# Optimization experiments

Measured on AMD Instinct MI355X. Metric: run time of the kernel, lower is better.

The kernel has to match this reference:

```python
import jax, jax.numpy as jnp
import numpy as np

B, S, K = 4, 2048, 8
N_NEURONS, N_BASIS, RANK = 64, 32, 8
D_MODEL, D_HID = 256, 1024


def setup_inputs() -> dict:
    key = jax.random.key(0)
    ks = jax.random.split(key, 10)
    x = jax.random.normal(ks[0], (B, S, D_MODEL), dtype=jnp.float32)
    neuron_idx = jax.random.randint(ks[1], (B, S, K), 0, N_NEURONS)
    w = jax.random.uniform(ks[2], (B, S, K), dtype=jnp.float32)
    neuron_weights = w / jnp.sum(w, axis=-1, keepdims=True)  # softmax-like routing weights
    neuron_recipes = jax.random.normal(ks[3], (N_NEURONS, N_BASIS), dtype=jnp.float32) * 0.5
    sc = 0.1
    basis_A1 = jax.random.normal(ks[4], (N_BASIS, 16, RANK, 8), dtype=jnp.float32) * sc
    basis_A2 = jax.random.normal(ks[5], (N_BASIS, RANK, 16, 8), dtype=jnp.float32) * sc
    basis_B1 = jax.random.normal(ks[6], (N_BASIS, 8, RANK, 32), dtype=jnp.float32) * sc
    basis_B2 = jax.random.normal(ks[7], (N_BASIS, RANK, 8, 32), dtype=jnp.float32) * sc
    w_down_w = jax.random.normal(ks[8], (D_HID, D_MODEL), dtype=jnp.float32) * (1.0 / np.sqrt(D_HID))
    w_down_b = jnp.zeros((D_MODEL,), dtype=jnp.float32)
    return {
        "x": x, "neuron_idx": neuron_idx, "neuron_weights": neuron_weights,
        "neuron_recipes": neuron_recipes,
        "basis_A1": basis_A1, "basis_A2": basis_A2,
        "basis_B1": basis_B1, "basis_B2": basis_B2,
        "w_down_w": w_down_w, "w_down_b": w_down_b,
    }


def reference(x, neuron_idx, neuron_weights, neuron_recipes,
              basis_A1, basis_A2, basis_B1, basis_B2, w_down_w, w_down_b):
    Bt, St, D = x.shape
    # --- routing: gather recipes of selected neurons, softmax, weighted-combine ---
    sel = neuron_recipes[neuron_idx]                       # [B,S,k,n_basis]
    sel = jax.nn.softmax(sel, axis=-1)
    wr = jnp.einsum('bskn,bsk->bsn', sel, neuron_weights)  # [B,S,n_basis]
    # --- build per-token TT cores from basis banks (get_neuron_tt_cores) ---
    cA1 = jnp.einsum('bsn,nirk->bsirk', wr, basis_A1)      # [B,S,16,r,8]
    cA2 = jnp.einsum('bsn,nrjl->bsrjl', wr, basis_A2)      # [B,S,r,16,8]
    cB1 = jnp.einsum('bsn,nirk->bsirk', wr, basis_B1)      # [B,S,8,r,32]
    cB2 = jnp.einsum('bsn,nrjl->bsrjl', wr, basis_B2)      # [B,S,r,8,32]
    # --- TT FFN: 256 -> 64 ---
    x_fold = x.reshape(Bt, St, 16, 16)
    temp = jnp.einsum('bsij,bsirk->bsjrk', x_fold, cA1)
    h = jnp.einsum('bsjrk,bsrjl->bskl', temp, cA2).reshape(Bt, St, 64)
    # --- TT FFN: 64 -> 1024 ---
    h_fold = h.reshape(Bt, St, 8, 8)
    temp = jnp.einsum('bsij,bsirk->bsjrk', h_fold, cB1)
    out = jnp.einsum('bsjrk,bsrjl->bskl', temp, cB2).reshape(Bt, St, D_HID)
    out = jax.nn.gelu(out, approximate=False)              # torch F.gelu default = exact erf
    return out @ w_down_w + w_down_b                       # [B,S,256]
```

## Files before the change

### kernel.cpp

```cpp
#include <hip/hip_runtime.h>
#include <math.h>


typedef unsigned short u16;
typedef __attribute__((ext_vector_type(8))) __bf16 bf16x8;
typedef __attribute__((ext_vector_type(4))) float f32x4;
union ABCast { float4 f; bf16x8 v; };
union BFBits { __bf16 b; u16 u; };
union Pack8 { u16 u[8]; float4 f; };

__device__ __forceinline__ float gelu_exact(float v) {
    return 0.5f * v * (1.0f + erff(v * 0.70710678118654752440f));
}
__device__ __forceinline__ u16 f2bf_bits(float f) { BFBits c; c.b = (__bf16)f; return c.u; }
__device__ __forceinline__ float bfbits2f(u16 u) { BFBits c; c.u = u; return (float)c.b; }

__global__ __launch_bounds__(64) void k_route(
    const int* __restrict__ nidx, const float* __restrict__ nw,
    const float* __restrict__ recipes, float* __restrict__ wr_out,
    u16* __restrict__ wrAh, u16* __restrict__ wrAl)
{
    const int t = blockIdx.x * 64 + threadIdx.x;
    float acc[32];
#pragma unroll
    for (int n = 0; n < 32; n++) acc[n] = 0.f;
#pragma unroll
    for (int k = 0; k < 8; k++) {
        const int   id = nidx[t * 8 + k];
        const float wk = nw[t * 8 + k];
        const float4* row = (const float4*)(recipes + id * 32);
        float v[32];
#pragma unroll
        for (int q = 0; q < 8; q++) {
            float4 f = row[q];
            v[q*4+0] = f.x; v[q*4+1] = f.y; v[q*4+2] = f.z; v[q*4+3] = f.w;
        }
        float m = v[0];
#pragma unroll
        for (int n = 1; n < 32; n++) m = fmaxf(m, v[n]);
        float s = 0.f;
#pragma unroll
        for (int n = 0; n < 32; n++) { float e = expf(v[n] - m); v[n] = e; s += e; }
        const float iv = wk / s;
#pragma unroll
        for (int n = 0; n < 32; n++) acc[n] += v[n] * iv;
    }
    float4* o = (float4*)(wr_out + t * 32);
#pragma unroll
    for (int q = 0; q < 8; q++)
        o[q] = make_float4(acc[q*4+0], acc[q*4+1], acc[q*4+2], acc[q*4+3]);

    const int tg16 = t >> 4, tl = t & 15;
#pragma unroll
    for (int c = 0; c < 4; c++) {
        Pack8 ph, pl;
#pragma unroll
        for (int e = 0; e < 8; e++) {
            const float v = acc[c*8 + e];
            const u16 hb = f2bf_bits(v);
            ph.u[e] = hb;
            pl.u[e] = f2bf_bits(v - bfbits2f(hb));
        }
        const int lane = c * 16 + tl;
        *(float4*)(wrAh + (tg16*64 + lane)*8) = ph.f;
        *(float4*)(wrAl + (tg16*64 + lane)*8) = pl.f;
    }
}

__global__ __launch_bounds__(512) void k_stageA(
    const float* __restrict__ x, const float* __restrict__ wr,
    const float* __restrict__ A1, const float* __restrict__ A2,
    float* __restrict__ h_out)
{
    __shared__ float ca[8 * 1024];
    __shared__ float tl[8 * 1088];
    const int tid = threadIdx.x;
    const int t0  = blockIdx.x * 8;
    {
        const int e2 = tid * 2;
        float2 c[8];
#pragma unroll
        for (int tt = 0; tt < 8; tt++) c[tt] = make_float2(0.f, 0.f);
#pragma unroll 4
        for (int n = 0; n < 32; n++) {
            const float2 a = *(const float2*)(A1 + n * 1024 + e2);
#pragma unroll
            for (int tt = 0; tt < 8; tt++) {
                const float s = wr[(t0 + tt) * 32 + n];
                c[tt].x += s * a.x; c[tt].y += s * a.y;
            }
        }
#pragma unroll
        for (int tt = 0; tt < 8; tt++) *(float2*)(ca + tt * 1024 + e2) = c[tt];
    }
    __syncthreads();
    {
        const int t = tid >> 6, g = tid & 63, j = g >> 2, eh = g & 3;
        float xr[16];
#pragma unroll
        for (int i = 0; i < 16; i++) xr[i] = x[(t0 + t) * 256 + i * 16 + j];
        float tr[16];
#pragma unroll
        for (int q = 0; q < 16; q++) tr[q] = 0.f;
#pragma unroll
        for (int i = 0; i < 16; i++) {
            const float xv = xr[i];
#pragma unroll
            for (int q = 0; q < 4; q++) {
                const float4 cv = *(const float4*)(ca + t * 1024 + i * 64 + eh * 16 + q * 4);
                tr[q*4+0] += xv * cv.x; tr[q*4+1] += xv * cv.y;
                tr[q*4+2] += xv * cv.z; tr[q*4+3] += xv * cv.w;
            }
        }
#pragma unroll
        for (int q = 0; q < 4; q++)
            *(float4*)(tl + t * 1088 + j * 68 + eh * 16 + q * 4) =
                make_float4(tr[q*4+0], tr[q*4+1], tr[q*4+2], tr[q*4+3]);
    }
    __syncthreads();
    {
        const int e2 = tid * 2;
        float2 c[8];
#pragma unroll
        for (int tt = 0; tt < 8; tt++) c[tt] = make_float2(0.f, 0.f);
#pragma unroll 4
        for (int n = 0; n < 32; n++) {
            const float2 a = *(const float2*)(A2 + n * 1024 + e2);
#pragma unroll
            for (int tt = 0; tt < 8; tt++) {
                const float s = wr[(t0 + tt) * 32 + n];
                c[tt].x += s * a.x; c[tt].y += s * a.y;
            }
        }
#pragma unroll
        for (int tt = 0; tt < 8; tt++) *(float2*)(ca + tt * 1024 + e2) = c[tt];
    }
    __syncthreads();
    {
        const int t = tid >> 6, g = tid & 63, k = g >> 3, l = g & 7;
        float acc = 0.f;
#pragma unroll
        for (int j = 0; j < 16; j++) {
#pragma unroll
            for (int r = 0; r < 8; r++) {
                acc += tl[t * 1088 + j * 68 + r * 8 + k] *
                       ca[t * 1024 + r * 128 + j * 8 + l];
            }
        }
        h_out[(t0 + t) * 64 + g] = acc;
    }
}

__global__ __launch_bounds__(256) void k_bsplit(
    const float* __restrict__ B1, const float* __restrict__ B2,
    u16* __restrict__ o1h, u16* __restrict__ o1l,
    u16* __restrict__ o2h, u16* __restrict__ o2l)
{
    const int slot = blockIdx.x * 256 + threadIdx.x;
    const int bank = slot >> 13, r = (slot >> 10) & 7, g = (slot >> 6) & 15, l = slot & 63;
    const int c = l & 15, nb = 8 * (l >> 4);
    const int base = (bank == 0)
        ? ((g >> 1) * 256 + r * 32 + (g & 1) * 16 + c)
        : (r * 256 + (g >> 1) * 32 + (g & 1) * 16 + c);
    const float* S = (bank ? B2 : B1) + base + nb * 2048;
    Pack8 ph, pl;
#pragma unroll
    for (int e = 0; e < 8; e++) {
        const float v = S[e * 2048];
        const u16 hb = f2bf_bits(v);
        ph.u[e] = hb;
        pl.u[e] = f2bf_bits(v - bfbits2f(hb));
    }
    const int d = ((r * 16 + g) * 64 + l) * 8;
    *(float4*)((bank ? o2h : o1h) + d) = ph.f;
    *(float4*)((bank ? o2l : o1l) + d) = pl.f;
}

__global__ __launch_bounds__(256) void k_wsplit(
    const float* __restrict__ W, u16* __restrict__ wfh, u16* __restrict__ wfl)
{
    const int slot = blockIdx.x * 256 + threadIdx.x;
    const int ng = slot >> 11, kc = (slot >> 6) & 31, l = slot & 63;
    const float* S = W + (kc * 32 + 8 * (l >> 4)) * 256 + ng * 16 + (l & 15);
    Pack8 ph, pl;
#pragma unroll
    for (int e = 0; e < 8; e++) {
        const float v = S[e * 256];
        const u16 hb = f2bf_bits(v);
        ph.u[e] = hb;
        pl.u[e] = f2bf_bits(v - bfbits2f(hb));
    }
    const int d = ((ng * 32 + kc) * 64 + l) * 8;
    *(float4*)(wfh + d) = ph.f;
    *(float4*)(wfl + d) = pl.f;
}

__global__ __launch_bounds__(1024, 2) void k_fusedB(
    const float* __restrict__ hin,
    const u16* __restrict__ wrAh, const u16* __restrict__ wrAl,
    const u16* __restrict__ bf1h, const u16* __restrict__ bf1l,
    const u16* __restrict__ bf2h, const u16* __restrict__ bf2l,
    const u16* __restrict__ wfh, const u16* __restrict__ wfl,
    const float* __restrict__ bias, float* __restrict__ y)
{
    __shared__ __align__(16) unsigned char smem[65536];
    float* hs  = (float*)smem;
    float* cb1 = hs + 1024;
    float* cb2 = cb1 + 16 * 264;
    float* t2  = cb2 + 16 * 264;
    u16* gAh = (u16*)smem;
    u16* gAl = gAh + 16384;

    const int tid = threadIdx.x;
    const int l   = tid & 63;
    const int w   = tid >> 6;
    const int tg  = blockIdx.x;
    const int t0  = tg * 16;

    hs[tid] = hin[t0 * 64 + tid];

    ABCast cu;
    cu.f = *(const float4*)(wrAh + (tg * 64 + l) * 8); const bf16x8 wra_h = cu.v;
    cu.f = *(const float4*)(wrAl + (tg * 64 + l) * 8); const bf16x8 wra_l = cu.v;

    const bool isB2 = (w >= 8);
    const u16* bsrc_h = isB2 ? bf2h : bf1h;
    const u16* bsrc_l = isB2 ? bf2l : bf1l;
    float* cdst = isB2 ? cb2 : cb1;
    const int g0 = (w & 7) * 2;

    const int j2 = l >> 3, k42 = l & 7;
    const int k0 = (l & 7) * 4, l0 = (l >> 3) * 4;

    float hreg[8];
#pragma unroll
    for (int i = 0; i < 8; i++) hreg[i] = hs[w * 64 + i * 8 + j2];

    float o[4][4];
#pragma unroll
    for (int a = 0; a < 4; a++)
#pragma unroll
        for (int li = 0; li < 4; li++) o[a][li] = 0.f;

    float4 pbh0 = *(const float4*)(bsrc_h + ((g0 + 0)*64 + l)*8);
    float4 pbl0 = *(const float4*)(bsrc_l + ((g0 + 0)*64 + l)*8);
    float4 pbh1 = *(const float4*)(bsrc_h + ((g0 + 1)*64 + l)*8);
    float4 pbl1 = *(const float4*)(bsrc_l + ((g0 + 1)*64 + l)*8);

#pragma unroll 1
    for (int r = 0; r < 8; r++) {
        {
            ABCast ch, cl2;
            ch.f = pbh0; cl2.f = pbl0;
            f32x4 cc = {0.f, 0.f, 0.f, 0.f};
            cc = __builtin_amdgcn_mfma_f32_16x16x32_bf16(wra_h, ch.v,  cc, 0, 0, 0);
            cc = __builtin_amdgcn_mfma_f32_16x16x32_bf16(wra_h, cl2.v, cc, 0, 0, 0);
            cc = __builtin_amdgcn_mfma_f32_16x16x32_bf16(wra_l, ch.v,  cc, 0, 0, 0);
            {
                const int gg = g0;
                float* cd = cdst + (gg >> 1) * 32 + (gg & 1) * 16 + (l & 15);
#pragma unroll
                for (int reg = 0; reg < 4; reg++)
                    cd[(4 * (l >> 4) + reg) * 264] = cc[reg];
            }
            ch.f = pbh1; cl2.f = pbl1;
            f32x4 cc2 = {0.f, 0.f, 0.f, 0.f};
            cc2 = __builtin_amdgcn_mfma_f32_16x16x32_bf16(wra_h, ch.v,  cc2, 0, 0, 0);
            cc2 = __builtin_amdgcn_mfma_f32_16x16x32_bf16(wra_h, cl2.v, cc2, 0, 0, 0);
            cc2 = __builtin_amdgcn_mfma_f32_16x16x32_bf16(wra_l, ch.v,  cc2, 0, 0, 0);
            {
                const int gg = g0 + 1;
                float* cd = cdst + (gg >> 1) * 32 + (gg & 1) * 16 + (l & 15);
#pragma unroll
                for (int reg = 0; reg < 4; reg++)
                    cd[(4 * (l >> 4) + reg) * 264] = cc2[reg];
            }
        }
        if (r < 7) {
            const int rb = (r + 1) * 16;
            pbh0 = *(const float4*)(bsrc_h + ((rb + g0 + 0)*64 + l)*8);
            pbl0 = *(const float4*)(bsrc_l + ((rb + g0 + 0)*64 + l)*8);
            pbh1 = *(const float4*)(bsrc_h + ((rb + g0 + 1)*64 + l)*8);
            pbl1 = *(const float4*)(bsrc_l + ((rb + g0 + 1)*64 + l)*8);
        }
        __syncthreads();

        {
            float4 acc = make_float4(0.f, 0.f, 0.f, 0.f);
#pragma unroll
            for (int i = 0; i < 8; i++) {
                const float  hv = hreg[i];
                const float4 cv = *(const float4*)(cb1 + w * 264 + i * 32 + k42 * 4);
                acc.x += hv * cv.x; acc.y += hv * cv.y;
                acc.z += hv * cv.z; acc.w += hv * cv.w;
            }
            *(float4*)(t2 + w * 264 + j2 * 32 + k42 * 4) = acc;
        }

        {
#pragma unroll
            for (int j = 0; j < 8; j++) {
                const float4 tv4 = *(const float4*)(t2  + w * 264 + j * 32 + k0);
                const float4 cv4 = *(const float4*)(cb2 + w * 264 + j * 32 + l0);
                const float tv[4] = {tv4.x, tv4.y, tv4.z, tv4.w};
                const float cv[4] = {cv4.x, cv4.y, cv4.z, cv4.w};
#pragma unroll
                for (int a = 0; a < 4; a++)
#pragma unroll
                    for (int li = 0; li < 4; li++)
                        o[a][li] += tv[a] * cv[li];
            }
        }
        __syncthreads();
    }

    {
        const int lane2 = (l0 >> 3) * 16 + w;
        const int e0 = l0 & 7;
#pragma unroll
        for (int a = 0; a < 4; a++) {
            u16 hv[4], lv[4];
#pragma unroll
            for (int li = 0; li < 4; li++) {
                const float v = gelu_exact(o[a][li]);
                const u16 hb = f2bf_bits(v);
                hv[li] = hb;
                lv[li] = f2bf_bits(v - bfbits2f(hb));
            }
            const int step = k0 + a;
            *(ushort4*)(gAh + (step * 64 + lane2) * 8 + e0) = make_ushort4(hv[0], hv[1], hv[2], hv[3]);
            *(ushort4*)(gAl + (step * 64 + lane2) * 8 + e0) = make_ushort4(lv[0], lv[1], lv[2], lv[3]);
        }
    }
    __syncthreads();

    if (w < 8) {
        f32x4 dacc0 = {0.f, 0.f, 0.f, 0.f}, dacc1 = {0.f, 0.f, 0.f, 0.f};
        const int wb0 = w * 16384 + l * 8;
        const int wb1 = (w + 8) * 16384 + l * 8;
#pragma unroll 2
        for (int kc = 0; kc < 32; kc++) {
            cu.f = *(const float4*)(gAh + (kc * 64 + l) * 8); const bf16x8 ah = cu.v;
            cu.f = *(const float4*)(gAl + (kc * 64 + l) * 8); const bf16x8 al = cu.v;
            ABCast c0, c1, c2, c3;
            c0.f = *(const float4*)(wfh + wb0 + kc * 512); const bf16x8 bh0 = c0.v;
            c1.f = *(const float4*)(wfl + wb0 + kc * 512); const bf16x8 bl0 = c1.v;
            c2.f = *(const float4*)(wfh + wb1 + kc * 512); const bf16x8 bh1 = c2.v;
            c3.f = *(const float4*)(wfl + wb1 + kc * 512); const bf16x8 bl1 = c3.v;
            dacc0 = __builtin_amdgcn_mfma_f32_16x16x32_bf16(ah, bh0, dacc0, 0, 0, 0);
            dacc0 = __builtin_amdgcn_mfma_f32_16x16x32_bf16(ah, bl0, dacc0, 0, 0, 0);
            dacc0 = __builtin_amdgcn_mfma_f32_16x16x32_bf16(al, bh0, dacc0, 0, 0, 0);
            dacc1 = __builtin_amdgcn_mfma_f32_16x16x32_bf16(ah, bh1, dacc1, 0, 0, 0);
            dacc1 = __builtin_amdgcn_mfma_f32_16x16x32_bf16(ah, bl1, dacc1, 0, 0, 0);
            dacc1 = __builtin_amdgcn_mfma_f32_16x16x32_bf16(al, bh1, dacc1, 0, 0, 0);
        }
        const int n0 = w * 16 + (l & 15);
        const int n1 = (w + 8) * 16 + (l & 15);
        const float b0 = bias[n0], b1 = bias[n1];
        const int tb = t0 + 4 * (l >> 4);
#pragma unroll
        for (int reg = 0; reg < 4; reg++) {
            y[(tb + reg) * 256 + n0] = dacc0[reg] + b0;
            y[(tb + reg) * 256 + n1] = dacc1[reg] + b1;
        }
    }
}

extern "C" void kernel_launch(void* const* d_in, const int* in_sizes, int n_in,
                              void* d_out, int out_size, void* d_ws, size_t ws_size,
                              hipStream_t stream)
{
    const float* x    = (const float*)d_in[0];
    const int*   nidx = (const int*)  d_in[1];
    const float* nw   = (const float*)d_in[2];
    const float* rec  = (const float*)d_in[3];
    const float* A1   = (const float*)d_in[4];
    const float* A2   = (const float*)d_in[5];
    const float* B1   = (const float*)d_in[6];
    const float* B2   = (const float*)d_in[7];
    const float* Wd   = (const float*)d_in[8];
    const float* bd   = (const float*)d_in[9];
    float* y  = (float*)d_out;

    float* wr  = (float*)d_ws;
    float* h   = wr + 8192 * 32;
    u16* wrAh  = (u16*)(h + 8192 * 64);
    u16* wrAl  = wrAh + 262144;
    u16* b1h   = wrAl + 262144;
    u16* b1l   = b1h + 65536;
    u16* b2h   = b1l + 65536;
    u16* b2l   = b2h + 65536;
    u16* wfh   = b2l + 65536;
    u16* wfl   = wfh + 262144;

    k_route <<<128,  64,   0, stream>>>(nidx, nw, rec, wr, wrAh, wrAl);
    k_stageA<<<1024, 512,  0, stream>>>(x, wr, A1, A2, h);
    k_bsplit<<<64,   256,  0, stream>>>(B1, B2, b1h, b1l, b2h, b2l);
    k_wsplit<<<128,  256,  0, stream>>>(Wd, wfh, wfl);
    k_fusedB<<<512,  1024, 0, stream>>>(h, wrAh, wrAl, b1h, b1l, b2h, b2l, wfh, wfl, bd, y);
}
```

Measured before the change: 101.1 us.

## Double-buffer TT core build and compute t2 in registers to drop a barrier

Core tiles cb1/cb2 are now double-buffered in shared memory, so the MFMA build of the next rank slice overlaps with the contraction on the current one, leaving one barrier per iteration instead of two. The t2 intermediate is no longer staged through shared memory: each thread recomputes the full 8x4 slice it needs in registers from a per-wave copy of h held in 64 registers. This raises register pressure and redundant FMAs under launch_bounds(1024,2) and grows shared memory past 64KB, which may cost occupancy or cause spills.

```diff
diff --git a/kernel.cpp b/kernel.cpp
--- a/kernel.cpp
+++ b/kernel.cpp
@@ -203,11 +203,9 @@
     const u16* __restrict__ wfh, const u16* __restrict__ wfl,
     const float* __restrict__ bias, float* __restrict__ y)
 {
-    __shared__ __align__(16) unsigned char smem[65536];
-    float* hs  = (float*)smem;
-    float* cb1 = hs + 1024;
-    float* cb2 = cb1 + 16 * 264;
-    float* t2  = cb2 + 16 * 264;
+    __shared__ __align__(16) unsigned char smem[67584];
+    float* cb1 = (float*)smem;
+    float* cb2 = cb1 + 2 * 16 * 264;
     u16* gAh = (u16*)smem;
     u16* gAl = gAh + 16384;
 
@@ -217,7 +215,11 @@
     const int tg  = blockIdx.x;
     const int t0  = tg * 16;
 
-    hs[tid] = hin[t0 * 64 + tid];
+    const int wu = __builtin_amdgcn_readfirstlane(w);
+    const float* hp = hin + (t0 + wu) * 64;
+    float hsg[64];
+#pragma unroll
+    for (int q = 0; q < 64; q++) hsg[q] = hp[q];
 
     ABCast cu;
     cu.f = *(const float4*)(wrAh + (tg * 64 + l) * 8); const bf16x8 wra_h = cu.v;
@@ -226,93 +228,92 @@
     const bool isB2 = (w >= 8);
     const u16* bsrc_h = isB2 ? bf2h : bf1h;
     const u16* bsrc_l = isB2 ? bf2l : bf1l;
-    float* cdst = isB2 ? cb2 : cb1;
+    float* cdst0 = isB2 ? cb2 : cb1;
     const int g0 = (w & 7) * 2;
 
-    const int j2 = l >> 3, k42 = l & 7;
     const int k0 = (l & 7) * 4, l0 = (l >> 3) * 4;
 
-    float hreg[8];
-#pragma unroll
-    for (int i = 0; i < 8; i++) hreg[i] = hs[w * 64 + i * 8 + j2];
-
     float o[4][4];
 #pragma unroll
     for (int a = 0; a < 4; a++)
 #pragma unroll
         for (int li = 0; li < 4; li++) o[a][li] = 0.f;
 
-    float4 pbh0 = *(const float4*)(bsrc_h + ((g0 + 0)*64 + l)*8);
-    float4 pbl0 = *(const float4*)(bsrc_l + ((g0 + 0)*64 + l)*8);
-    float4 pbh1 = *(const float4*)(bsrc_h + ((g0 + 1)*64 + l)*8);
-    float4 pbl1 = *(const float4*)(bsrc_l + ((g0 + 1)*64 + l)*8);
+    float4 pbh0, pbl0, pbh1, pbl1;
+#define LOADB(R) {                                                              \
+    const int rb_ = (R) * 16;                                                   \
+    pbh0 = *(const float4*)(bsrc_h + ((rb_ + g0 + 0)*64 + l)*8);                \
+    pbl0 = *(const float4*)(bsrc_l + ((rb_ + g0 + 0)*64 + l)*8);                \
+    pbh1 = *(const float4*)(bsrc_h + ((rb_ + g0 + 1)*64 + l)*8);                \
+    pbl1 = *(const float4*)(bsrc_l + ((rb_ + g0 + 1)*64 + l)*8); }
+#define BUILD(BSEL) {                                                           \
+    float* cdst = cdst0 + (BSEL) * 4224;                                        \
+    ABCast ch_, cl_;                                                            \
+    ch_.f = pbh0; cl_.f = pbl0;                                                 \
+    f32x4 cc = {0.f, 0.f, 0.f, 0.f};                                            \
+    cc = __builtin_amdgcn_mfma_f32_16x16x32_bf16(wra_h, ch_.v, cc, 0, 0, 0);    \
+    cc = __builtin_amdgcn_mfma_f32_16x16x32_bf16(wra_h, cl_.v, cc, 0, 0, 0);    \
+    cc = __builtin_amdgcn_mfma_f32_16x16x32_bf16(wra_l, ch_.v, cc, 0, 0, 0);    \
+    { const int gg = g0;                                                        \
+      float* cd = cdst + (gg >> 1) * 32 + (gg & 1) * 16 + (l & 15);             \
+      _Pragma("unroll")                                                         \
+      for (int reg = 0; reg < 4; reg++) cd[(4 * (l >> 4) + reg) * 264] = cc[reg]; } \
+    ch_.f = pbh1; cl_.f = pbl1;                                                 \
+    f32x4 cc2 = {0.f, 0.f, 0.f, 0.f};                                           \
+    cc2 = __builtin_amdgcn_mfma_f32_16x16x32_bf16(wra_h, ch_.v, cc2, 0, 0, 0);  \
+    cc2 = __builtin_amdgcn_mfma_f32_16x16x32_bf16(wra_h, cl_.v, cc2, 0, 0, 0);  \
+    cc2 = __builtin_amdgcn_mfma_f32_16x16x32_bf16(wra_l, ch_.v, cc2, 0, 0, 0);  \
+    { const int gg = g0 + 1;                                                    \
+      float* cd = cdst + (gg >> 1) * 32 + (gg & 1) * 16 + (l & 15);             \
+      _Pragma("unroll")                                                         \
+      for (int reg = 0; reg < 4; reg++) cd[(4 * (l >> 4) + reg) * 264] = cc2[reg]; } }
+
+    LOADB(0);
+    BUILD(0);
+    LOADB(1);
+    __syncthreads();
 
 #pragma unroll 1
     for (int r = 0; r < 8; r++) {
+        if (r < 7) {
+            BUILD((r + 1) & 1);
+            if (r < 6) LOADB(r + 2);
+        }
+
         {
-            ABCast ch, cl2;
-            ch.f = pbh0; cl2.f = pbl0;
-            f32x4 cc = {0.f, 0.f, 0.f, 0.f};
-            cc = __builtin_amdgcn_mfma_f32_16x16x32_bf16(wra_h, ch.v,  cc, 0, 0, 0);
-            cc = __builtin_amdgcn_mfma_f32_16x16x32_bf16(wra_h, cl2.v, cc, 0, 0, 0);
-            cc = __builtin_amdgcn_mfma_f32_16x16x32_bf16(wra_l, ch.v,  cc, 0, 0, 0);
-            {
-                const int gg = g0;
-                float* cd = cdst + (gg >> 1) * 32 + (gg & 1) * 16 + (l & 15);
-#pragma unroll
-                for (int reg = 0; reg < 4; reg++)
-                    cd[(4 * (l >> 4) + reg) * 264] = cc[reg];
-            }
-            ch.f = pbh1; cl2.f = pbl1;
-            f32x4 cc2 = {0.f, 0.f, 0.f, 0.f};
-            cc2 = __builtin_amdgcn_mfma_f32_16x16x32_bf16(wra_h, ch.v,  cc2, 0, 0, 0);
-            cc2 = __builtin_amdgcn_mfma_f32_16x16x32_bf16(wra_h, cl2.v, cc2, 0, 0, 0);
-            cc2 = __builtin_amdgcn_mfma_f32_16x16x32_bf16(wra_l, ch.v,  cc2, 0, 0, 0);
-            {
-                const int gg = g0 + 1;
-                float* cd = cdst + (gg >> 1) * 32 + (gg & 1) * 16 + (l & 15);
-#pragma unroll
-                for (int reg = 0; reg < 4; reg++)
-                    cd[(4 * (l >> 4) + reg) * 264] = cc2[reg];
-            }
-        }
-        if (r < 7) {
-            const int rb = (r + 1) * 16;
-            pbh0 = *(const float4*)(bsrc_h + ((rb + g0 + 0)*64 + l)*8);
-            pbl0 = *(const float4*)(bsrc_l + ((rb + g0 + 0)*64 + l)*8);
-            pbh1 = *(const float4*)(bsrc_h + ((rb + g0 + 1)*64 + l)*8);
-            pbl1 = *(const float4*)(bsrc_l + ((rb + g0 + 1)*64 + l)*8);
+            const float* c1b = cb1 + (r & 1) * 4224 + w * 264;
+            const float* c2b = cb2 + (r & 1) * 4224 + w * 264;
+            float t2q[8][4];
+#pragma unroll
+            for (int j = 0; j < 8; j++)
+#pragma unroll
+                for (int a = 0; a < 4; a++) t2q[j][a] = 0.f;
+#pragma unroll
+            for (int i = 0; i < 8; i++) {
+                const float4 c1 = *(const float4*)(c1b + i * 32 + k0);
+                const float cv[4] = {c1.x, c1.y, c1.z, c1.w};
+#pragma unroll
+                for (int j = 0; j < 8; j++) {
+                    const float hv = hsg[i * 8 + j];
+#pragma unroll
+                    for (int a = 0; a < 4; a++) t2q[j][a] += hv * cv[a];
+                }
+            }
+#pragma unroll
+            for (int j = 0; j < 8; j++) {
+                const float4 c2 = *(const float4*)(c2b + j * 32 + l0);
+                const float cv[4] = {c2.x, c2.y, c2.z, c2.w};
+#pragma unroll
+                for (int a = 0; a < 4; a++)
+#pragma unroll
+                    for (int li = 0; li < 4; li++)
+                        o[a][li] += t2q[j][a] * cv[li];
+            }
         }
         __syncthreads();
-
-        {
-            float4 acc = make_float4(0.f, 0.f, 0.f, 0.f);
-#pragma unroll
-            for (int i = 0; i < 8; i++) {
-                const float  hv = hreg[i];
-                const float4 cv = *(const float4*)(cb1 + w * 264 + i * 32 + k42 * 4);
-                acc.x += hv * cv.x; acc.y += hv * cv.y;
-                acc.z += hv * cv.z; acc.w += hv * cv.w;
-            }
-            *(float4*)(t2 + w * 264 + j2 * 32 + k42 * 4) = acc;
-        }
-
-        {
-#pragma unroll
-            for (int j = 0; j < 8; j++) {
-                const float4 tv4 = *(const float4*)(t2  + w * 264 + j * 32 + k0);
-                const float4 cv4 = *(const float4*)(cb2 + w * 264 + j * 32 + l0);
-                const float tv[4] = {tv4.x, tv4.y, tv4.z, tv4.w};
-                const float cv[4] = {cv4.x, cv4.y, cv4.z, cv4.w};
-#pragma unroll
-                for (int a = 0; a < 4; a++)
-#pragma unroll
-                    for (int li = 0; li < 4; li++)
-                        o[a][li] += tv[a] * cv[li];
-            }
-        }
-        __syncthreads();
-    }
+    }
+#undef LOADB
+#undef BUILD
 
     {
         const int lane2 = (l0 >> 3) * 16 + w;
```

Result: slower. 138.6 us (+37.0%).
